# Kernel tuning notes

Hardware: AMD Instinct MI355X
Metric: run time of the kernel (lower is better)

## Reference

```python
import jax, jax.numpy as jnp
import numpy as np

B, T, IN_DIM, H = 128, 512, 128, 512


def _lstm_layer(x, W_ih, W_hh, b_ih, b_hh):
    """Single-layer batch-first LSTM (PyTorch gate order i,f,g,o).
    x: [B, T, D]. Returns (outputs [B, T, H], h_T [B, H], c_T [B, H])."""
    Bsz = x.shape[0]
    Hdim = W_hh.shape[1]
    # Precompute the input contribution for all timesteps: [T, B, 4H]
    xg = jnp.einsum('btd,gd->tbg', x, W_ih) + (b_ih + b_hh)

    def step(carry, xg_t):
        h, c = carry
        gates = xg_t + h @ W_hh.T  # [B, 4H]
        i, f, g, o = jnp.split(gates, 4, axis=-1)
        i = jax.nn.sigmoid(i)
        f = jax.nn.sigmoid(f)
        g = jnp.tanh(g)
        o = jax.nn.sigmoid(o)
        c = f * c + i * g
        h = o * jnp.tanh(c)
        return (h, c), h

    h0 = jnp.zeros((Bsz, Hdim), dtype=x.dtype)
    c0 = jnp.zeros((Bsz, Hdim), dtype=x.dtype)
    (hT, cT), outs = jax.lax.scan(step, (h0, c0), xg)
    return jnp.transpose(outs, (1, 0, 2)), hT, cT


def setup_inputs() -> dict:
    key = jax.random.key(0)
    ks = jax.random.split(key, 9)
    s1 = 1.0 / np.sqrt(H)
    inp = {
        'x': jax.random.normal(ks[0], (B, T, IN_DIM), dtype=jnp.float32),
        'W_ih1': jax.random.uniform(ks[1], (4 * H, IN_DIM), jnp.float32, -s1, s1),
        'W_hh1': jax.random.uniform(ks[2], (4 * H, H), jnp.float32, -s1, s1),
        'b_ih1': jax.random.uniform(ks[3], (4 * H,), jnp.float32, -s1, s1),
        'b_hh1': jax.random.uniform(ks[4], (4 * H,), jnp.float32, -s1, s1),
        'W_ih2': jax.random.uniform(ks[5], (4 * H, H), jnp.float32, -s1, s1),
        'W_hh2': jax.random.uniform(ks[6], (4 * H, H), jnp.float32, -s1, s1),
        'b_ih2': jax.random.uniform(ks[7], (4 * H,), jnp.float32, -s1, s1),
        'b_hh2': jax.random.uniform(ks[8], (4 * H,), jnp.float32, -s1, s1),
    }
    return inp


def reference(x, W_ih1, W_hh1, b_ih1, b_hh1, W_ih2, W_hh2, b_ih2, b_hh2):
    out1, _, _ = _lstm_layer(x, W_ih1, W_hh1, b_ih1, b_hh1)
    _, hT, cT = _lstm_layer(out1, W_ih2, W_hh2, b_ih2, b_hh2)
    # Match torch nn.LSTM final-state shape: [num_layers*dirs=1, B, H]
    return hT[None, :, :], cT[None, :, :]
```

## Files before the change

### kernel.cpp

```cpp
#include <hip/hip_runtime.h>
#include <stdint.h>
#include <stddef.h>


typedef __attribute__((ext_vector_type(8))) short short8;
typedef __attribute__((ext_vector_type(4))) float f32x4;
typedef unsigned long long u64;

#define DEV static __device__ __forceinline__
#define SCOPE_AGENT __HIP_MEMORY_SCOPE_AGENT

constexpr int TSEQ = 512;
constexpr int DIN  = 128;
constexpr int HDIM = 512;
constexpr int NCL  = 8;
constexpr int BB   = 16;
constexpr int NJ   = 32;
constexpr int COLS = 16;

DEV unsigned short f2bf(float f) {
  unsigned u = __float_as_uint(f);
  u += 0x7fffu + ((u >> 16) & 1u);
  return (unsigned short)(u >> 16);
}
DEV short8 pack8(float4 a, float4 b) {
  short8 r;
  r[0] = (short)f2bf(a.x); r[1] = (short)f2bf(a.y);
  r[2] = (short)f2bf(a.z); r[3] = (short)f2bf(a.w);
  r[4] = (short)f2bf(b.x); r[5] = (short)f2bf(b.y);
  r[6] = (short)f2bf(b.z); r[7] = (short)f2bf(b.w);
  return r;
}
DEV short8 mk8(u64 lo, u64 hi) {
  union { u64 q[2]; short8 v; } u;
  u.q[0] = lo; u.q[1] = hi; return u.v;
}
DEV f32x4 mfma16(short8 a, short8 b, f32x4 c) {
  return __builtin_amdgcn_mfma_f32_16x16x32_bf16(a, b, c, 0, 0, 0);
}
DEV float sigf(float v) { return 1.f / (1.f + __expf(-v)); }
DEV float tanh_(float v) {
  v = fminf(20.f, fmaxf(-20.f, v));
  float e = __expf(2.f * v);
  return (e - 1.f) / (e + 1.f);
}

__global__ void zero_ws(unsigned* p, int n) {
  int i = blockIdx.x * 256 + threadIdx.x;
  if (i < n)
    __hip_atomic_store(p + i, 0u, __ATOMIC_RELAXED, SCOPE_AGENT);
}

#define SWZ(row, idx) ((idx) ^ (((row) & 15) << 3))

__global__ __launch_bounds__(256, 1) void lstm_persist(
    const float* __restrict__ x,
    const float* __restrict__ Wih1, const float* __restrict__ Whh1,
    const float* __restrict__ bih1, const float* __restrict__ bhh1,
    const float* __restrict__ Wih2, const float* __restrict__ Whh2,
    const float* __restrict__ bih2, const float* __restrict__ bhh2,
    float* __restrict__ out,
    unsigned short* __restrict__ buf1,
    unsigned short* __restrict__ buf2,
    unsigned* __restrict__ flags)
{
  __shared__ short xs [16 * DIN];
  __shared__ short h1s[16 * HDIM];
  __shared__ short h2s[16 * HDIM];
  __shared__ float red1[4 * 16 * 66];
  __shared__ float red2[4 * 16 * 66];
  __shared__ float bias1s[64], bias2s[64];
  __shared__ float occpad[3072];

  const int tid  = threadIdx.x;
  const int lane = tid & 63;
  const int lm   = lane & 15;
  const int lq   = lane >> 4;
  const int kq   = tid >> 6;

  const int bid     = blockIdx.x;
  const int cluster = bid & 7;
  const int j       = bid >> 3;
  const int cb      = cluster * BB;

  asm volatile("" :: "v"(&occpad[tid & 1023]));

  short8 wf1[4][5];
  short8 wf2[4][8];
  #pragma unroll
  for (int g = 0; g < 4; ++g) {
    const int gr = g * HDIM + j * COLS + lm;
    #pragma unroll
    for (int sl = 0; sl < 5; ++sl) {
      const int k0 = (kq * 5 + sl) * 32 + 8 * lq;
      const float* src = (k0 < DIN) ? (Wih1 + (size_t)gr * DIN + k0)
                                    : (Whh1 + (size_t)gr * HDIM + (k0 - DIN));
      wf1[g][sl] = pack8(*(const float4*)src, *(const float4*)(src + 4));
    }
    #pragma unroll
    for (int sl = 0; sl < 8; ++sl) {
      const int k0 = (kq * 8 + sl) * 32 + 8 * lq;
      const float* src = (k0 < HDIM) ? (Wih2 + (size_t)gr * HDIM + k0)
                                     : (Whh2 + (size_t)gr * HDIM + (k0 - HDIM));
      wf2[g][sl] = pack8(*(const float4*)src, *(const float4*)(src + 4));
    }
  }
  if (tid < 64) {
    const int g = tid >> 4, nn = tid & 15;
    const int gr = g * HDIM + j * COLS + nn;
    bias1s[tid] = bih1[gr] + bhh1[gr];
    bias2s[tid] = bih2[gr] + bhh2[gr];
  }

  const int pm = tid >> 4, pnn = tid & 15;
  float c1 = 0.f, c2 = 0.f;

  for (int it = 0; it <= TSEQ; ++it) {
    const bool l1 = (it < TSEQ);
    const bool l2 = (it >= 1);

    if (l1) {
      const int row = tid >> 4, kc = tid & 15;
      const float* xp = x + ((size_t)(cb + row) * TSEQ + it) * DIN + kc * 8;
      *(short8*)(&xs[SWZ(row, row * DIN + kc * 8)]) =
          pack8(*(const float4*)xp, *(const float4*)(xp + 4));
    }

    if (it > 0) {
      if (kq == 0) {
        const unsigned* fl = flags + cluster * 64 + lane;
        const unsigned tgt = (lane < NJ) ? (unsigned)it : (unsigned)(it - 1);
        while (true) {
          unsigned v = __hip_atomic_load(fl, __ATOMIC_RELAXED, SCOPE_AGENT);
          if (__all((int)(v >= tgt))) break;
          __builtin_amdgcn_s_sleep(1);
        }
      }
      __syncthreads();
    }

    const unsigned short* h1r =
        buf1 + (size_t)(((it + 1) & 1) * NCL + cluster) * BB * HDIM;
    const unsigned short* h2r =
        buf2 + (size_t)((it & 1) * NCL + cluster) * BB * HDIM;
    {
      u64 t[8];
      #pragma unroll
      for (int ci = 0; ci < 4; ++ci) {
        const int c = ci * 256 + tid;
        const int row = c >> 6, kc = c & 63;
        const u64* s = (const u64*)(h1r + (size_t)row * HDIM + kc * 8);
        t[2 * ci]     = __hip_atomic_load(s,     __ATOMIC_RELAXED, SCOPE_AGENT);
        t[2 * ci + 1] = __hip_atomic_load(s + 1, __ATOMIC_RELAXED, SCOPE_AGENT);
      }
      #pragma unroll
      for (int ci = 0; ci < 4; ++ci) {
        const int c = ci * 256 + tid;
        const int row = c >> 6, kc = c & 63;
        u64* d = (u64*)&h1s[SWZ(row, row * HDIM + kc * 8)];
        d[0] = t[2 * ci]; d[1] = t[2 * ci + 1];
      }
      #pragma unroll
      for (int ci = 0; ci < 4; ++ci) {
        const int c = ci * 256 + tid;
        const int row = c >> 6, kc = c & 63;
        const u64* s = (const u64*)(h2r + (size_t)row * HDIM + kc * 8);
        t[2 * ci]     = __hip_atomic_load(s,     __ATOMIC_RELAXED, SCOPE_AGENT);
        t[2 * ci + 1] = __hip_atomic_load(s + 1, __ATOMIC_RELAXED, SCOPE_AGENT);
      }
      #pragma unroll
      for (int ci = 0; ci < 4; ++ci) {
        const int c = ci * 256 + tid;
        const int row = c >> 6, kc = c & 63;
        u64* d = (u64*)&h2s[SWZ(row, row * HDIM + kc * 8)];
        d[0] = t[2 * ci]; d[1] = t[2 * ci + 1];
      }
    }
    __syncthreads();

    f32x4 z = {0.f, 0.f, 0.f, 0.f};
    f32x4 acc1[4] = {z, z, z, z};
    f32x4 acc2[4] = {z, z, z, z};
    if (l1) {
      #pragma unroll
      for (int sl = 0; sl < 5; ++sl) {
        const int s = kq * 5 + sl;
        short8 a;
        if (s < 4)
          a = *(const short8*)(&xs[SWZ(lm, lm * DIN + s * 32 + 8 * lq)]);
        else
          a = *(const short8*)(&h1s[SWZ(lm, lm * HDIM + (s - 4) * 32 + 8 * lq)]);
        #pragma unroll
        for (int g = 0; g < 4; ++g) acc1[g] = mfma16(a, wf1[g][sl], acc1[g]);
      }
    }
    if (l2) {
      #pragma unroll
      for (int sl = 0; sl < 8; ++sl) {
        const int s2 = kq * 8 + sl;
        short8 a;
        if (s2 < 16)
          a = *(const short8*)(&h1s[SWZ(lm, lm * HDIM + s2 * 32 + 8 * lq)]);
        else
          a = *(const short8*)(&h2s[SWZ(lm, lm * HDIM + (s2 - 16) * 32 + 8 * lq)]);
        #pragma unroll
        for (int g = 0; g < 4; ++g) acc2[g] = mfma16(a, wf2[g][sl], acc2[g]);
      }
    }
    if (l1) {
      #pragma unroll
      for (int g = 0; g < 4; ++g)
        #pragma unroll
        for (int r = 0; r < 4; ++r)
          red1[(kq * 16 + lq * 4 + r) * 66 + g * 16 + lm] = acc1[g][r];
    }
    if (l2) {
      #pragma unroll
      for (int g = 0; g < 4; ++g)
        #pragma unroll
        for (int r = 0; r < 4; ++r)
          red2[(kq * 16 + lq * 4 + r) * 66 + g * 16 + lm] = acc2[g][r];
    }
    __syncthreads();

    if (l1) {
      float p[4];
      #pragma unroll
      for (int g = 0; g < 4; ++g) {
        float v = bias1s[g * 16 + pnn];
        #pragma unroll
        for (int q = 0; q < 4; ++q) v += red1[(q * 16 + pm) * 66 + g * 16 + pnn];
        p[g] = v;
      }
      const float i_ = sigf(p[0]), f_ = sigf(p[1]);
      const float g_ = tanh_(p[2]), o_ = sigf(p[3]);
      c1 = f_ * c1 + i_ * g_;
      const float h1v = o_ * tanh_(c1);
      unsigned short* wp = buf1 + (size_t)((it & 1) * NCL + cluster) * BB * HDIM;
      __hip_atomic_store(&wp[pm * HDIM + j * COLS + pnn], f2bf(h1v),
                         __ATOMIC_RELAXED, SCOPE_AGENT);
    }
    __syncthreads();
    if (tid == 0 && l1)
      __hip_atomic_store(flags + cluster * 64 + j, (unsigned)(it + 1),
                         __ATOMIC_RELAXED, SCOPE_AGENT);

    if (l2) {
      float p[4];
      #pragma unroll
      for (int g = 0; g < 4; ++g) {
        float v = bias2s[g * 16 + pnn];
        #pragma unroll
        for (int q = 0; q < 4; ++q) v += red2[(q * 16 + pm) * 66 + g * 16 + pnn];
        p[g] = v;
      }
      const float i_ = sigf(p[0]), f_ = sigf(p[1]);
      const float g_ = tanh_(p[2]), o_ = sigf(p[3]);
      c2 = f_ * c2 + i_ * g_;
      const float h2v = o_ * tanh_(c2);
      if (l1) {
        unsigned short* wp =
            buf2 + (size_t)(((it + 1) & 1) * NCL + cluster) * BB * HDIM;
        __hip_atomic_store(&wp[pm * HDIM + j * COLS + pnn], f2bf(h2v),
                           __ATOMIC_RELAXED, SCOPE_AGENT);
      } else {
        const int b = cb + pm;
        out[(size_t)b * HDIM + j * COLS + pnn] = h2v;
        out[(size_t)128 * HDIM + (size_t)b * HDIM + j * COLS + pnn] = c2;
      }
    }
    __syncthreads();
    if (tid == 0 && l1 && l2)
      __hip_atomic_store(flags + cluster * 64 + NJ + j, (unsigned)it,
                         __ATOMIC_RELAXED, SCOPE_AGENT);
  }
}

extern "C" void kernel_launch(void* const* d_in, const int* in_sizes, int n_in,
                              void* d_out, int out_size, void* d_ws, size_t ws_size,
                              hipStream_t stream) {
  const float* x    = (const float*)d_in[0];
  const float* Wih1 = (const float*)d_in[1];
  const float* Whh1 = (const float*)d_in[2];
  const float* bih1 = (const float*)d_in[3];
  const float* bhh1 = (const float*)d_in[4];
  const float* Wih2 = (const float*)d_in[5];
  const float* Whh2 = (const float*)d_in[6];
  const float* bih2 = (const float*)d_in[7];
  const float* bhh2 = (const float*)d_in[8];
  float* out = (float*)d_out;

  const size_t bufElems = (size_t)2 * NCL * BB * HDIM;
  unsigned short* buf1 = (unsigned short*)d_ws;
  unsigned short* buf2 = buf1 + bufElems;
  unsigned* flags = (unsigned*)(buf2 + bufElems);

  const int nzero = (int)((bufElems * 2 * 2 + NCL * 64 * 4) / 4);
  zero_ws<<<(nzero + 255) / 256, 256, 0, stream>>>((unsigned*)d_ws, nzero);
  lstm_persist<<<256, 256, 0, stream>>>(x, Wih1, Whh1, bih1, bhh1,
                                        Wih2, Whh2, bih2, bhh2,
                                        out, buf1, buf2, flags);
}
```

Baseline: 1.986 ms.

## Skew layer-2 three steps behind layer-1 with a four-slot h1 ring

Layer 2 now runs three timesteps behind layer 1 and reads layer-1 outputs from a four-deep ring buffer in global memory, staged through a new o1s shared array. Layer-1 gates are computed, written and flagged before layer-2 work begins, so other blocks waiting on h1 can proceed earlier and layer 2 leaves the critical recurrence path. Global loads of x and o1 are issued before the spin-wait to hide latency, and the occupancy padding array is removed. The cost is two extra loop iterations, an additional __syncthreads per step, more workspace and more shared memory.

```diff
diff --git a/kernel.cpp b/kernel.cpp
--- a/kernel.cpp
+++ b/kernel.cpp
@@ -66,11 +66,11 @@
 {
   __shared__ short xs [16 * DIN];
   __shared__ short h1s[16 * HDIM];
+  __shared__ short o1s[16 * HDIM];
   __shared__ short h2s[16 * HDIM];
   __shared__ float red1[4 * 16 * 66];
   __shared__ float red2[4 * 16 * 66];
   __shared__ float bias1s[64], bias2s[64];
-  __shared__ float occpad[3072];
 
   const int tid  = threadIdx.x;
   const int lane = tid & 63;
@@ -82,8 +82,8 @@
   const int cluster = bid & 7;
   const int j       = bid >> 3;
   const int cb      = cluster * BB;
-
-  asm volatile("" :: "v"(&occpad[tid & 1023]));
+  unsigned* flagA = flags + cluster * 64;
+  unsigned* flagB = flags + cluster * 64 + NJ;
 
   short8 wf1[4][5];
   short8 wf2[4][8];
@@ -115,21 +115,36 @@
   const int pm = tid >> 4, pnn = tid & 15;
   float c1 = 0.f, c2 = 0.f;
 
-  for (int it = 0; it <= TSEQ; ++it) {
+  for (int it = 0; it <= TSEQ + 2; ++it) {
     const bool l1 = (it < TSEQ);
-    const bool l2 = (it >= 1);
-
+    const bool l2 = (it >= 3);
+    const int  t2 = it - 3;
+
+    float4 xa, xb;
     if (l1) {
       const int row = tid >> 4, kc = tid & 15;
       const float* xp = x + ((size_t)(cb + row) * TSEQ + it) * DIN + kc * 8;
-      *(short8*)(&xs[SWZ(row, row * DIN + kc * 8)]) =
-          pack8(*(const float4*)xp, *(const float4*)(xp + 4));
+      xa = *(const float4*)xp; xb = *(const float4*)(xp + 4);
+    }
+    u64 o1t[8];
+    if (l2) {
+      const unsigned short* o1r =
+          buf1 + (size_t)(((t2 & 3) * NCL + cluster) * BB) * HDIM;
+      #pragma unroll
+      for (int ci = 0; ci < 4; ++ci) {
+        const int g = ci * 256 + tid, row = g >> 6, kc = g & 63;
+        const u64* s = (const u64*)(o1r + (size_t)row * HDIM + kc * 8);
+        o1t[2 * ci]     = __hip_atomic_load(s,     __ATOMIC_RELAXED, SCOPE_AGENT);
+        o1t[2 * ci + 1] = __hip_atomic_load(s + 1, __ATOMIC_RELAXED, SCOPE_AGENT);
+      }
     }
 
     if (it > 0) {
       if (kq == 0) {
-        const unsigned* fl = flags + cluster * 64 + lane;
-        const unsigned tgt = (lane < NJ) ? (unsigned)it : (unsigned)(it - 1);
+        const unsigned tgtA = (unsigned)(l1 ? it : TSEQ);
+        const unsigned tgtB = (it >= 4) ? (unsigned)(it - 1) : 0u;
+        const unsigned tgt  = (lane < NJ) ? tgtA : tgtB;
+        const unsigned* fl  = flagA + lane;
         while (true) {
           unsigned v = __hip_atomic_load(fl, __ATOMIC_RELAXED, SCOPE_AGENT);
           if (__all((int)(v >= tgt))) break;
@@ -139,49 +154,64 @@
       __syncthreads();
     }
 
-    const unsigned short* h1r =
-        buf1 + (size_t)(((it + 1) & 1) * NCL + cluster) * BB * HDIM;
-    const unsigned short* h2r =
-        buf2 + (size_t)((it & 1) * NCL + cluster) * BB * HDIM;
+    if (l1) {
+      const int row = tid >> 4, kc = tid & 15;
+      *(short8*)(&xs[SWZ(row, row * DIN + kc * 8)]) = pack8(xa, xb);
+    }
+    if (l2) {
+      #pragma unroll
+      for (int ci = 0; ci < 4; ++ci) {
+        const int g = ci * 256 + tid, row = g >> 6, kc = g & 63;
+        *(short8*)(&o1s[SWZ(row, row * HDIM + kc * 8)]) =
+            mk8(o1t[2 * ci], o1t[2 * ci + 1]);
+      }
+    }
     {
-      u64 t[8];
-      #pragma unroll
-      for (int ci = 0; ci < 4; ++ci) {
-        const int c = ci * 256 + tid;
-        const int row = c >> 6, kc = c & 63;
-        const u64* s = (const u64*)(h1r + (size_t)row * HDIM + kc * 8);
-        t[2 * ci]     = __hip_atomic_load(s,     __ATOMIC_RELAXED, SCOPE_AGENT);
-        t[2 * ci + 1] = __hip_atomic_load(s + 1, __ATOMIC_RELAXED, SCOPE_AGENT);
-      }
-      #pragma unroll
-      for (int ci = 0; ci < 4; ++ci) {
-        const int c = ci * 256 + tid;
-        const int row = c >> 6, kc = c & 63;
-        u64* d = (u64*)&h1s[SWZ(row, row * HDIM + kc * 8)];
-        d[0] = t[2 * ci]; d[1] = t[2 * ci + 1];
-      }
-      #pragma unroll
-      for (int ci = 0; ci < 4; ++ci) {
-        const int c = ci * 256 + tid;
-        const int row = c >> 6, kc = c & 63;
-        const u64* s = (const u64*)(h2r + (size_t)row * HDIM + kc * 8);
-        t[2 * ci]     = __hip_atomic_load(s,     __ATOMIC_RELAXED, SCOPE_AGENT);
-        t[2 * ci + 1] = __hip_atomic_load(s + 1, __ATOMIC_RELAXED, SCOPE_AGENT);
-      }
-      #pragma unroll
-      for (int ci = 0; ci < 4; ++ci) {
-        const int c = ci * 256 + tid;
-        const int row = c >> 6, kc = c & 63;
-        u64* d = (u64*)&h2s[SWZ(row, row * HDIM + kc * 8)];
-        d[0] = t[2 * ci]; d[1] = t[2 * ci + 1];
-      }
-    }
-    __syncthreads();
-
-    f32x4 z = {0.f, 0.f, 0.f, 0.f};
-    f32x4 acc1[4] = {z, z, z, z};
-    f32x4 acc2[4] = {z, z, z, z};
+      u64 h1t[8], h2t[8];
+      const unsigned short* h1r =
+          buf1 + (size_t)((((it + 3) & 3) * NCL + cluster) * BB) * HDIM;
+      const unsigned short* h2r =
+          buf2 + (size_t)(((it & 1) * NCL + cluster) * BB) * HDIM;
+      if (l1) {
+        #pragma unroll
+        for (int ci = 0; ci < 4; ++ci) {
+          const int g = ci * 256 + tid, row = g >> 6, kc = g & 63;
+          const u64* s = (const u64*)(h1r + (size_t)row * HDIM + kc * 8);
+          h1t[2 * ci]     = __hip_atomic_load(s,     __ATOMIC_RELAXED, SCOPE_AGENT);
+          h1t[2 * ci + 1] = __hip_atomic_load(s + 1, __ATOMIC_RELAXED, SCOPE_AGENT);
+        }
+      }
+      if (l2) {
+        #pragma unroll
+        for (int ci = 0; ci < 4; ++ci) {
+          const int g = ci * 256 + tid, row = g >> 6, kc = g & 63;
+          const u64* s = (const u64*)(h2r + (size_t)row * HDIM + kc * 8);
+          h2t[2 * ci]     = __hip_atomic_load(s,     __ATOMIC_RELAXED, SCOPE_AGENT);
+          h2t[2 * ci + 1] = __hip_atomic_load(s + 1, __ATOMIC_RELAXED, SCOPE_AGENT);
+        }
+      }
+      if (l1) {
+        #pragma unroll
+        for (int ci = 0; ci < 4; ++ci) {
+          const int g = ci * 256 + tid, row = g >> 6, kc = g & 63;
+          *(short8*)(&h1s[SWZ(row, row * HDIM + kc * 8)]) =
+              mk8(h1t[2 * ci], h1t[2 * ci + 1]);
+        }
+      }
+      if (l2) {
+        #pragma unroll
+        for (int ci = 0; ci < 4; ++ci) {
+          const int g = ci * 256 + tid, row = g >> 6, kc = g & 63;
+          *(short8*)(&h2s[SWZ(row, row * HDIM + kc * 8)]) =
+              mk8(h2t[2 * ci], h2t[2 * ci + 1]);
+        }
+      }
+    }
+    __syncthreads();
+
     if (l1) {
+      f32x4 z = {0.f, 0.f, 0.f, 0.f};
+      f32x4 acc1[4] = {z, z, z, z};
       #pragma unroll
       for (int sl = 0; sl < 5; ++sl) {
         const int s = kq * 5 + sl;
@@ -193,28 +223,50 @@
         #pragma unroll
         for (int g = 0; g < 4; ++g) acc1[g] = mfma16(a, wf1[g][sl], acc1[g]);
       }
-    }
+      #pragma unroll
+      for (int g = 0; g < 4; ++g)
+        #pragma unroll
+        for (int r = 0; r < 4; ++r)
+          red1[(kq * 16 + lq * 4 + r) * 66 + g * 16 + lm] = acc1[g][r];
+    }
+    __syncthreads();
+    if (l1) {
+      float p[4];
+      #pragma unroll
+      for (int g = 0; g < 4; ++g) {
+        float v = bias1s[g * 16 + pnn];
+        #pragma unroll
+        for (int q = 0; q < 4; ++q) v += red1[(q * 16 + pm) * 66 + g * 16 + pnn];
+        p[g] = v;
+      }
+      const float i_ = sigf(p[0]), f_ = sigf(p[1]);
+      const float g_ = tanh_(p[2]), o_ = sigf(p[3]);
+      c1 = f_ * c1 + i_ * g_;
+      const float h1v = o_ * tanh_(c1);
+      unsigned short* wp =
+          buf1 + (size_t)(((it & 3) * NCL + cluster) * BB) * HDIM;
+      __hip_atomic_store(&wp[pm * HDIM + j * COLS + pnn], f2bf(h1v),
+                         __ATOMIC_RELAXED, SCOPE_AGENT);
+    }
+    __syncthreads();
+    if (tid == 0 && l1)
+      __hip_atomic_store(flagA + j, (unsigned)(it + 1),
+                         __ATOMIC_RELAXED, SCOPE_AGENT);
+
     if (l2) {
+      f32x4 z = {0.f, 0.f, 0.f, 0.f};
+      f32x4 acc2[4] = {z, z, z, z};
       #pragma unroll
       for (int sl = 0; sl < 8; ++sl) {
         const int s2 = kq * 8 + sl;
         short8 a;
         if (s2 < 16)
-          a = *(const short8*)(&h1s[SWZ(lm, lm * HDIM + s2 * 32 + 8 * lq)]);
+          a = *(const short8*)(&o1s[SWZ(lm, lm * HDIM + s2 * 32 + 8 * lq)]);
         else
           a = *(const short8*)(&h2s[SWZ(lm, lm * HDIM + (s2 - 16) * 32 + 8 * lq)]);
         #pragma unroll
         for (int g = 0; g < 4; ++g) acc2[g] = mfma16(a, wf2[g][sl], acc2[g]);
       }
-    }
-    if (l1) {
-      #pragma unroll
-      for (int g = 0; g < 4; ++g)
-        #pragma unroll
-        for (int r = 0; r < 4; ++r)
-          red1[(kq * 16 + lq * 4 + r) * 66 + g * 16 + lm] = acc1[g][r];
-    }
-    if (l2) {
       #pragma unroll
       for (int g = 0; g < 4; ++g)
         #pragma unroll
@@ -222,29 +274,6 @@
           red2[(kq * 16 + lq * 4 + r) * 66 + g * 16 + lm] = acc2[g][r];
     }
     __syncthreads();
-
-    if (l1) {
-      float p[4];
-      #pragma unroll
-      for (int g = 0; g < 4; ++g) {
-        float v = bias1s[g * 16 + pnn];
-        #pragma unroll
-        for (int q = 0; q < 4; ++q) v += red1[(q * 16 + pm) * 66 + g * 16 + pnn];
-        p[g] = v;
-      }
-      const float i_ = sigf(p[0]), f_ = sigf(p[1]);
-      const float g_ = tanh_(p[2]), o_ = sigf(p[3]);
-      c1 = f_ * c1 + i_ * g_;
-      const float h1v = o_ * tanh_(c1);
-      unsigned short* wp = buf1 + (size_t)((it & 1) * NCL + cluster) * BB * HDIM;
-      __hip_atomic_store(&wp[pm * HDIM + j * COLS + pnn], f2bf(h1v),
-                         __ATOMIC_RELAXED, SCOPE_AGENT);
-    }
-    __syncthreads();
-    if (tid == 0 && l1)
-      __hip_atomic_store(flags + cluster * 64 + j, (unsigned)(it + 1),
-                         __ATOMIC_RELAXED, SCOPE_AGENT);
-
     if (l2) {
       float p[4];
       #pragma unroll
@@ -258,9 +287,9 @@
       const float g_ = tanh_(p[2]), o_ = sigf(p[3]);
       c2 = f_ * c2 + i_ * g_;
       const float h2v = o_ * tanh_(c2);
-      if (l1) {
+      if (t2 < TSEQ - 1) {
         unsigned short* wp =
-            buf2 + (size_t)(((it + 1) & 1) * NCL + cluster) * BB * HDIM;
+            buf2 + (size_t)((((it + 1) & 1) * NCL + cluster) * BB) * HDIM;
         __hip_atomic_store(&wp[pm * HDIM + j * COLS + pnn], f2bf(h2v),
                            __ATOMIC_RELAXED, SCOPE_AGENT);
       } else {
@@ -270,8 +299,8 @@
       }
     }
     __syncthreads();
-    if (tid == 0 && l1 && l2)
-      __hip_atomic_store(flags + cluster * 64 + NJ + j, (unsigned)it,
+    if (tid == 0 && l2)
+      __hip_atomic_store(flagB + j, (unsigned)it,
                          __ATOMIC_RELAXED, SCOPE_AGENT);
   }
 }
@@ -290,12 +319,13 @@
   const float* bhh2 = (const float*)d_in[8];
   float* out = (float*)d_out;
 
-  const size_t bufElems = (size_t)2 * NCL * BB * HDIM;
+  const size_t buf1Elems = (size_t)4 * NCL * BB * HDIM;
+  const size_t buf2Elems = (size_t)2 * NCL * BB * HDIM;
   unsigned short* buf1 = (unsigned short*)d_ws;
-  unsigned short* buf2 = buf1 + bufElems;
-  unsigned* flags = (unsigned*)(buf2 + bufElems);
-
-  const int nzero = (int)((bufElems * 2 * 2 + NCL * 64 * 4) / 4);
+  unsigned short* buf2 = buf1 + buf1Elems;
+  unsigned* flags = (unsigned*)(buf2 + buf2Elems);
+
+  const int nzero = (int)(((buf1Elems + buf2Elems) * 2 + NCL * 64 * 4) / 4);
   zero_ws<<<(nzero + 255) / 256, 256, 0, stream>>>((unsigned*)d_ws, nzero);
   lstm_persist<<<256, 256, 0, stream>>>(x, Wih1, Whh1, bih1, bhh1,
                                         Wih2, Whh2, bih2, bhh2,
```

New measurement: 1.982 ms. Within noise of the previous version (-0.2%).

## Per-thread flag polling on producer block, drop pre-load barrier, pad reduction stride

Applied to the files above, without the earlier changes.

Each thread now spins only on the flags of the producer block that wrote the h1/h2 column slice it loads. This replaces the single-wave poll followed by a block-wide barrier, so the exchange can start before every producer has finished. The x load is issued before the wait and packed into LDS afterwards to hide its latency. h-buffer loads are regrouped so each lane covers one column chunk across four rows, both layers' loads are issued before any LDS store, and the reduction row stride changes from 66 to 68 to alter bank mapping. The cost is more atomic polling traffic, since every thread now reads two flags, and a loss of the earlier point where the whole block was synchronized.

```diff
diff --git a/kernel.cpp b/kernel.cpp
--- a/kernel.cpp
+++ b/kernel.cpp
@@ -67,8 +67,8 @@
   __shared__ short xs [16 * DIN];
   __shared__ short h1s[16 * HDIM];
   __shared__ short h2s[16 * HDIM];
-  __shared__ float red1[4 * 16 * 66];
-  __shared__ float red2[4 * 16 * 66];
+  __shared__ float red1[4 * 16 * 68];
+  __shared__ float red2[4 * 16 * 68];
   __shared__ float bias1s[64], bias2s[64];
   __shared__ float occpad[3072];
 
@@ -82,6 +82,8 @@
   const int cluster = bid & 7;
   const int j       = bid >> 3;
   const int cb      = cluster * BB;
+  unsigned* flagA = flags + cluster * 64;
+  unsigned* flagB = flags + cluster * 64 + NJ;
 
   asm volatile("" :: "v"(&occpad[tid & 1023]));
 
@@ -115,66 +117,69 @@
   const int pm = tid >> 4, pnn = tid & 15;
   float c1 = 0.f, c2 = 0.f;
 
+  const int lr   = lane >> 4;
+  const int skc  = kq * 16 + (lane & 15);
+  const int prod = skc >> 1;
+
   for (int it = 0; it <= TSEQ; ++it) {
     const bool l1 = (it < TSEQ);
     const bool l2 = (it >= 1);
 
-    if (l1) {
-      const int row = tid >> 4, kc = tid & 15;
-      const float* xp = x + ((size_t)(cb + row) * TSEQ + it) * DIN + kc * 8;
-      *(short8*)(&xs[SWZ(row, row * DIN + kc * 8)]) =
-          pack8(*(const float4*)xp, *(const float4*)(xp + 4));
-    }
-
-    if (it > 0) {
-      if (kq == 0) {
-        const unsigned* fl = flags + cluster * 64 + lane;
-        const unsigned tgt = (lane < NJ) ? (unsigned)it : (unsigned)(it - 1);
-        while (true) {
-          unsigned v = __hip_atomic_load(fl, __ATOMIC_RELAXED, SCOPE_AGENT);
-          if (__all((int)(v >= tgt))) break;
-          __builtin_amdgcn_s_sleep(1);
-        }
-      }
-      __syncthreads();
+    float4 xa, xb;
+    if (l1) {
+      const int row = tid >> 4, kc16 = tid & 15;
+      const float* xp = x + ((size_t)(cb + row) * TSEQ + it) * DIN + kc16 * 8;
+      xa = *(const float4*)xp; xb = *(const float4*)(xp + 4);
     }
 
     const unsigned short* h1r =
         buf1 + (size_t)(((it + 1) & 1) * NCL + cluster) * BB * HDIM;
     const unsigned short* h2r =
         buf2 + (size_t)((it & 1) * NCL + cluster) * BB * HDIM;
+    if (it > 0) {
+      const unsigned tgA = (unsigned)(it < TSEQ ? it : TSEQ);
+      const unsigned tgB = (unsigned)(it - 1);
+      const unsigned* fA = flagA + prod;
+      const unsigned* fB = flagB + prod;
+      while (true) {
+        unsigned a = __hip_atomic_load(fA, __ATOMIC_RELAXED, SCOPE_AGENT);
+        unsigned b = __hip_atomic_load(fB, __ATOMIC_RELAXED, SCOPE_AGENT);
+        if (a >= tgA && b >= tgB) break;
+        __builtin_amdgcn_s_sleep(1);
+      }
+    }
     {
-      u64 t[8];
+      u64 t1[8], t2[8];
       #pragma unroll
       for (int ci = 0; ci < 4; ++ci) {
-        const int c = ci * 256 + tid;
-        const int row = c >> 6, kc = c & 63;
-        const u64* s = (const u64*)(h1r + (size_t)row * HDIM + kc * 8);
-        t[2 * ci]     = __hip_atomic_load(s,     __ATOMIC_RELAXED, SCOPE_AGENT);
-        t[2 * ci + 1] = __hip_atomic_load(s + 1, __ATOMIC_RELAXED, SCOPE_AGENT);
+        const int row = ci * 4 + lr;
+        const u64* s = (const u64*)(h1r + (size_t)row * HDIM + skc * 8);
+        t1[2 * ci]     = __hip_atomic_load(s,     __ATOMIC_RELAXED, SCOPE_AGENT);
+        t1[2 * ci + 1] = __hip_atomic_load(s + 1, __ATOMIC_RELAXED, SCOPE_AGENT);
       }
       #pragma unroll
       for (int ci = 0; ci < 4; ++ci) {
-        const int c = ci * 256 + tid;
-        const int row = c >> 6, kc = c & 63;
-        u64* d = (u64*)&h1s[SWZ(row, row * HDIM + kc * 8)];
-        d[0] = t[2 * ci]; d[1] = t[2 * ci + 1];
+        const int row = ci * 4 + lr;
+        const u64* s = (const u64*)(h2r + (size_t)row * HDIM + skc * 8);
+        t2[2 * ci]     = __hip_atomic_load(s,     __ATOMIC_RELAXED, SCOPE_AGENT);
+        t2[2 * ci + 1] = __hip_atomic_load(s + 1, __ATOMIC_RELAXED, SCOPE_AGENT);
       }
       #pragma unroll
       for (int ci = 0; ci < 4; ++ci) {
-        const int c = ci * 256 + tid;
-        const int row = c >> 6, kc = c & 63;
-        const u64* s = (const u64*)(h2r + (size_t)row * HDIM + kc * 8);
-        t[2 * ci]     = __hip_atomic_load(s,     __ATOMIC_RELAXED, SCOPE_AGENT);
-        t[2 * ci + 1] = __hip_atomic_load(s + 1, __ATOMIC_RELAXED, SCOPE_AGENT);
+        const int row = ci * 4 + lr;
+        *(short8*)(&h1s[SWZ(row, row * HDIM + skc * 8)]) =
+            mk8(t1[2 * ci], t1[2 * ci + 1]);
       }
       #pragma unroll
       for (int ci = 0; ci < 4; ++ci) {
-        const int c = ci * 256 + tid;
-        const int row = c >> 6, kc = c & 63;
-        u64* d = (u64*)&h2s[SWZ(row, row * HDIM + kc * 8)];
-        d[0] = t[2 * ci]; d[1] = t[2 * ci + 1];
-      }
+        const int row = ci * 4 + lr;
+        *(short8*)(&h2s[SWZ(row, row * HDIM + skc * 8)]) =
+            mk8(t2[2 * ci], t2[2 * ci + 1]);
+      }
+    }
+    if (l1) {
+      const int row = tid >> 4, kc16 = tid & 15;
+      *(short8*)(&xs[SWZ(row, row * DIN + kc16 * 8)]) = pack8(xa, xb);
     }
     __syncthreads();
 
@@ -212,14 +217,14 @@
       for (int g = 0; g < 4; ++g)
         #pragma unroll
         for (int r = 0; r < 4; ++r)
-          red1[(kq * 16 + lq * 4 + r) * 66 + g * 16 + lm] = acc1[g][r];
+          red1[(kq * 16 + lq * 4 + r) * 68 + g * 16 + lm] = acc1[g][r];
     }
     if (l2) {
       #pragma unroll
       for (int g = 0; g < 4; ++g)
         #pragma unroll
         for (int r = 0; r < 4; ++r)
-          red2[(kq * 16 + lq * 4 + r) * 66 + g * 16 + lm] = acc2[g][r];
+          red2[(kq * 16 + lq * 4 + r) * 68 + g * 16 + lm] = acc2[g][r];
     }
     __syncthreads();
 
@@ -229,7 +234,7 @@
       for (int g = 0; g < 4; ++g) {
         float v = bias1s[g * 16 + pnn];
         #pragma unroll
-        for (int q = 0; q < 4; ++q) v += red1[(q * 16 + pm) * 66 + g * 16 + pnn];
+        for (int q = 0; q < 4; ++q) v += red1[(q * 16 + pm) * 68 + g * 16 + pnn];
         p[g] = v;
       }
       const float i_ = sigf(p[0]), f_ = sigf(p[1]);
@@ -242,7 +247,7 @@
     }
     __syncthreads();
     if (tid == 0 && l1)
-      __hip_atomic_store(flags + cluster * 64 + j, (unsigned)(it + 1),
+      __hip_atomic_store(flagA + j, (unsigned)(it + 1),
                          __ATOMIC_RELAXED, SCOPE_AGENT);
 
     if (l2) {
@@ -251,7 +256,7 @@
       for (int g = 0; g < 4; ++g) {
         float v = bias2s[g * 16 + pnn];
         #pragma unroll
-        for (int q = 0; q < 4; ++q) v += red2[(q * 16 + pm) * 66 + g * 16 + pnn];
+        for (int q = 0; q < 4; ++q) v += red2[(q * 16 + pm) * 68 + g * 16 + pnn];
         p[g] = v;
       }
       const float i_ = sigf(p[0]), f_ = sigf(p[1]);
@@ -271,7 +276,7 @@
     }
     __syncthreads();
     if (tid == 0 && l1 && l2)
-      __hip_atomic_store(flags + cluster * 64 + NJ + j, (unsigned)it,
+      __hip_atomic_store(flagB + j, (unsigned)it,
                          __ATOMIC_RELAXED, SCOPE_AGENT);
   }
 }
```

Result: faster. 1.892 ms (-4.7%).
